# Optimization experiments

Hardware: AMD Instinct MI355X
Metric: run time of the kernel (lower is better)

## Reference

```python
import jax, jax.numpy as jnp
import numpy as np

IM_SIZE = (256, 256)
OVERSAMP = 1.25
WIDTH = 6
BETA = float(np.pi * np.sqrt((WIDTH / OVERSAMP * (OVERSAMP - 0.5)) ** 2 - 0.8))
OS_SIZE = tuple(int(np.ceil(OVERSAMP * n)) for n in IM_SIZE)  # (320, 320)
D = 2


def _kb(x):
    # Kaiser-Bessel interpolation kernel: i0(beta*sqrt(1-x^2)) for |x|<=1 (sigpy convention)
    return jnp.i0(BETA * jnp.sqrt(jnp.maximum(1.0 - x * x, 0.0)))


def setup_inputs() -> dict:
    key = jax.random.key(0)
    k1, k2, k3 = jax.random.split(key, 3)
    N, C = 1, 8
    img_r = jax.random.normal(k1, (N, C) + IM_SIZE, dtype=jnp.float32)
    img_i = jax.random.normal(k2, (N, C) + IM_SIZE, dtype=jnp.float32)
    # trajectory in [-N_i/2, N_i/2] per the class docstring
    trj = (jax.random.uniform(k3, (N, 64, 4096, D), dtype=jnp.float32) - 0.5) * 256.0
    return {"img_r": img_r, "img_i": img_i, "trj": trj}


def _nufft_forward(img_r, img_i, trj):
    img = (img_r + 1j * img_i).astype(jnp.complex64)  # (N, C, H, W)
    nd = img.ndim
    # --- apodization (inverse FT of KB kernel), separable per axis ---
    for a in range(D):
        n, osn = IM_SIZE[a], OS_SIZE[a]
        idx = jnp.arange(n, dtype=jnp.float32)
        arg = jnp.sqrt(BETA ** 2 - (np.pi * WIDTH * (idx - n // 2) / osn) ** 2)
        apod = arg / jnp.sinh(arg)
        shape = [1] * nd
        shape[nd - D + a] = n
        img = img * apod.reshape(shape)
    # --- scale + centered zero-pad to oversampled grid ---
    img = img / np.sqrt(float(np.prod(IM_SIZE)))
    pads = [(0, 0)] * (nd - D) + [(((o - n) // 2), (o - n) - ((o - n) // 2))
                                  for n, o in zip(IM_SIZE, OS_SIZE)]
    img = jnp.pad(img, pads)
    # --- centered FFT (ifftshift -> fftn(norm=None) -> fftshift) ---
    axes = tuple(range(-D, 0))
    ksp_os = jnp.fft.fftshift(jnp.fft.fftn(jnp.fft.ifftshift(img, axes=axes), axes=axes), axes=axes)
    # --- scale trajectory to oversampled grid coordinates ---
    scale = jnp.array([OS_SIZE[a] / IM_SIZE[a] for a in range(D)], jnp.float32)
    shift = jnp.array([OS_SIZE[a] // 2 for a in range(D)], jnp.float32)
    coord = trj * scale + shift  # (N, R, S, 2)
    x0 = jnp.ceil(coord - WIDTH / 2.0)
    # --- KB interpolation: fixed 6x6 neighbor loop, vectorized gather over all points ---
    N = img.shape[0]
    out = jnp.zeros((N,) + img.shape[1:nd - D] + coord.shape[1:-1], jnp.complex64)

    def gather(grid, ix, iy):  # grid (C, Hos, Wos), ix/iy (R, S) -> (C, R, S)
        return grid[:, ix, iy]

    for dx in range(WIDTH):
        px = x0[..., 0] + dx
        wx = _kb((px - coord[..., 0]) / (WIDTH / 2.0))
        ix = px.astype(jnp.int32) % OS_SIZE[0]
        for dy in range(WIDTH):
            py = x0[..., 1] + dy
            wy = _kb((py - coord[..., 1]) / (WIDTH / 2.0))
            iy = py.astype(jnp.int32) % OS_SIZE[1]
            vals = jax.vmap(gather)(ksp_os, ix, iy)  # (N, C, R, S)
            out = out + vals * (wx * wy)[:, None, :, :]
    return out / (WIDTH ** D)


def reference(img_r, img_i, trj):
    return _nufft_forward(img_r, img_i, trj)
```

## Files before the change

### kernel.cpp

```cpp
#include <hip/hip_runtime.h>
#include <math.h>

#define NCH   8
#define IMN   256
#define OSN   320
#define NPTS  (64*4096)
#define KD    512
#define BETA_F   10.9551078f
#define BETA2_F  120.014389f
#define APOD_C   0.05890486225f

typedef unsigned short u16;
typedef unsigned int   u32;
typedef __attribute__((ext_vector_type(8))) short s16x8;
typedef __attribute__((ext_vector_type(4))) float f32x4;
typedef __attribute__((ext_vector_type(2))) float f32x2;

__device__ __forceinline__ u32 f2bf(float f) {
    u32 u = __float_as_uint(f);
    return (u + 0x7FFFu + ((u >> 16) & 1u)) >> 16;
}

__device__ __forceinline__ float i0f(float t) {
    if (t < 3.75f) {
        float y = t * t * (1.0f / 14.0625f);
        return 1.0f + y * (3.5156229f + y * (3.0899424f + y * (1.2067492f +
                     y * (0.2659732f + y * (0.0360768f + y * 0.0045813f)))));
    }
    float z = 3.75f / t;
    float p = 0.39894228f + z * (0.01328592f + z * (0.00225319f + z * (-0.00157565f +
              z * (0.00916281f + z * (-0.02057706f + z * (0.02635537f +
              z * (-0.01647633f + z * 0.00392377f)))))));
    return expf(t) * rsqrtf(t) * p;
}

__device__ __forceinline__ float apodf(int i) {
    float x = APOD_C * (float)(i - IMN / 2);
    float arg = sqrtf(BETA2_F - x * x);
    float e = expf(arg);
    float sh = 0.5f * (e - 1.0f / e);
    return arg / sh;
}

__global__ void prep(const float* __restrict__ r, const float* __restrict__ im,
                     u32* __restrict__ B1, u32* __restrict__ B2,
                     u32* __restrict__ A) {
    const int b = blockIdx.x, t = threadIdx.x;
    if (b < (OSN * IMN) / 256) {
        int idx = b * 256 + t;
        int k = idx >> 8, j = idx & 255;
        int p = (k * (j + 32)) % OSN;
        float th = (2.0f * (float)M_PI / (float)OSN) * (float)p;
        float s = ((k + j) & 1) ? -1.0f : 1.0f;
        float sn, cs;
        sincosf(th, &sn, &cs);
        float re = s * cs, imv = -s * sn;
        B1[idx] = f2bf(re) | (f2bf(-imv) << 16);
        B2[idx] = f2bf(imv) | (f2bf(re) << 16);
    } else {
        int idx = (b - (OSN * IMN) / 256) * 256 + t;
        int i2 = idx & 255, i1 = (idx >> 8) & 255;
        float w = apodf(i1) * apodf(i2) * (1.0f / 256.0f);
        A[idx] = f2bf(r[idx] * w) | (f2bf(im[idx] * w) << 16);
    }
}

__launch_bounds__(64)
__global__ void gemm1(const short* __restrict__ Abf, const short* __restrict__ B1,
                      const short* __restrict__ B2, short* __restrict__ Tb) {
    const int c = blockIdx.z;
    const int mBase = blockIdx.y * 32;
    const int nBase = blockIdx.x * 32;
    __shared__ short As[2][32][36], B1s[2][32][36], B2s[2][32][36];
    const int t = threadIdx.x;
    const int row = t >> 1, seg = (t & 1) * 16;
    const int fm = t & 15, fq = (t >> 4) * 8;
    const short* ap  = Abf + (long)(c * IMN + mBase + row) * KD + seg;
    const short* b1p = B1 + (long)(nBase + row) * KD + seg;
    const short* b2p = B2 + (long)(nBase + row) * KD + seg;
    f32x4 zz = {0.f, 0.f, 0.f, 0.f};
    f32x4 accRe[2][2], accIm[2][2];
    #pragma unroll
    for (int i = 0; i < 2; i++)
        #pragma unroll
        for (int j = 0; j < 2; j++) { accRe[i][j] = zz; accIm[i][j] = zz; }

    s16x8 c0 = *(const s16x8*)(ap);
    s16x8 c1 = *(const s16x8*)(ap + 8);
    s16x8 c2 = *(const s16x8*)(b1p);
    s16x8 c3 = *(const s16x8*)(b1p + 8);
    s16x8 c4 = *(const s16x8*)(b2p);
    s16x8 c5 = *(const s16x8*)(b2p + 8);

    #pragma unroll
    for (int kc = 0; kc < 16; kc++) {
        const int buf = kc & 1;
        *(s16x8*)&As [buf][row][seg]     = c0;
        *(s16x8*)&As [buf][row][seg + 8] = c1;
        *(s16x8*)&B1s[buf][row][seg]     = c2;
        *(s16x8*)&B1s[buf][row][seg + 8] = c3;
        *(s16x8*)&B2s[buf][row][seg]     = c4;
        *(s16x8*)&B2s[buf][row][seg + 8] = c5;
        if (kc < 15) {
            const int kb = (kc + 1) * 32;
            c0 = *(const s16x8*)(ap + kb);
            c1 = *(const s16x8*)(ap + kb + 8);
            c2 = *(const s16x8*)(b1p + kb);
            c3 = *(const s16x8*)(b1p + kb + 8);
            c4 = *(const s16x8*)(b2p + kb);
            c5 = *(const s16x8*)(b2p + kb + 8);
        }
        s16x8 a0  = *(const s16x8*)&As [buf][fm][fq];
        s16x8 a1  = *(const s16x8*)&As [buf][16 + fm][fq];
        s16x8 b10 = *(const s16x8*)&B1s[buf][fm][fq];
        s16x8 b11 = *(const s16x8*)&B1s[buf][16 + fm][fq];
        s16x8 b20 = *(const s16x8*)&B2s[buf][fm][fq];
        s16x8 b21 = *(const s16x8*)&B2s[buf][16 + fm][fq];
        accRe[0][0] = __builtin_amdgcn_mfma_f32_16x16x32_bf16(a0, b10, accRe[0][0], 0, 0, 0);
        accRe[0][1] = __builtin_amdgcn_mfma_f32_16x16x32_bf16(a0, b11, accRe[0][1], 0, 0, 0);
        accRe[1][0] = __builtin_amdgcn_mfma_f32_16x16x32_bf16(a1, b10, accRe[1][0], 0, 0, 0);
        accRe[1][1] = __builtin_amdgcn_mfma_f32_16x16x32_bf16(a1, b11, accRe[1][1], 0, 0, 0);
        accIm[0][0] = __builtin_amdgcn_mfma_f32_16x16x32_bf16(a0, b20, accIm[0][0], 0, 0, 0);
        accIm[0][1] = __builtin_amdgcn_mfma_f32_16x16x32_bf16(a0, b21, accIm[0][1], 0, 0, 0);
        accIm[1][0] = __builtin_amdgcn_mfma_f32_16x16x32_bf16(a1, b20, accIm[1][0], 0, 0, 0);
        accIm[1][1] = __builtin_amdgcn_mfma_f32_16x16x32_bf16(a1, b21, accIm[1][1], 0, 0, 0);
    }
    #pragma unroll
    for (int i = 0; i < 2; i++)
        #pragma unroll
        for (int j = 0; j < 2; j++) {
            int i1b = mBase + i * 16 + (t >> 4) * 4;
            int k2  = nBase + j * 16 + fm;
            s16x8 v;
            #pragma unroll
            for (int r = 0; r < 4; r++) {
                v[2 * r]     = (short)f2bf(accRe[i][j][r]);
                v[2 * r + 1] = (short)f2bf(accIm[i][j][r]);
            }
            *(s16x8*)(Tb + ((long)(c * OSN + k2)) * KD + 2 * i1b) = v;
        }
}

__launch_bounds__(64)
__global__ void gemm2(const short* __restrict__ B1, const short* __restrict__ B2,
                      const short* __restrict__ Tb, u32* __restrict__ Gb) {
    const int c = blockIdx.z;
    const int mBase = blockIdx.y * 32;
    const int nBase = blockIdx.x * 32;
    __shared__ short A1s[2][32][36], A2s[2][32][36], Bs[2][32][36];
    const int t = threadIdx.x;
    const int row = t >> 1, seg = (t & 1) * 16;
    const int fm = t & 15, fq = (t >> 4) * 8;
    const short* a1p = B1 + (long)(mBase + row) * KD + seg;
    const short* a2p = B2 + (long)(mBase + row) * KD + seg;
    const short* bp  = Tb + ((long)(c * OSN + nBase + row)) * KD + seg;
    f32x4 zz = {0.f, 0.f, 0.f, 0.f};
    f32x4 accRe[2][2], accIm[2][2];
    #pragma unroll
    for (int i = 0; i < 2; i++)
        #pragma unroll
        for (int j = 0; j < 2; j++) { accRe[i][j] = zz; accIm[i][j] = zz; }

    s16x8 c0 = *(const s16x8*)(a1p);
    s16x8 c1 = *(const s16x8*)(a1p + 8);
    s16x8 c2 = *(const s16x8*)(a2p);
    s16x8 c3 = *(const s16x8*)(a2p + 8);
    s16x8 c4 = *(const s16x8*)(bp);
    s16x8 c5 = *(const s16x8*)(bp + 8);

    #pragma unroll
    for (int kc = 0; kc < 16; kc++) {
        const int buf = kc & 1;
        *(s16x8*)&A1s[buf][row][seg]     = c0;
        *(s16x8*)&A1s[buf][row][seg + 8] = c1;
        *(s16x8*)&A2s[buf][row][seg]     = c2;
        *(s16x8*)&A2s[buf][row][seg + 8] = c3;
        *(s16x8*)&Bs [buf][row][seg]     = c4;
        *(s16x8*)&Bs [buf][row][seg + 8] = c5;
        if (kc < 15) {
            const int kb = (kc + 1) * 32;
            c0 = *(const s16x8*)(a1p + kb);
            c1 = *(const s16x8*)(a1p + kb + 8);
            c2 = *(const s16x8*)(a2p + kb);
            c3 = *(const s16x8*)(a2p + kb + 8);
            c4 = *(const s16x8*)(bp + kb);
            c5 = *(const s16x8*)(bp + kb + 8);
        }
        s16x8 a10 = *(const s16x8*)&A1s[buf][fm][fq];
        s16x8 a11 = *(const s16x8*)&A1s[buf][16 + fm][fq];
        s16x8 a20 = *(const s16x8*)&A2s[buf][fm][fq];
        s16x8 a21 = *(const s16x8*)&A2s[buf][16 + fm][fq];
        s16x8 b0  = *(const s16x8*)&Bs [buf][fm][fq];
        s16x8 b1  = *(const s16x8*)&Bs [buf][16 + fm][fq];
        accRe[0][0] = __builtin_amdgcn_mfma_f32_16x16x32_bf16(a10, b0, accRe[0][0], 0, 0, 0);
        accRe[0][1] = __builtin_amdgcn_mfma_f32_16x16x32_bf16(a10, b1, accRe[0][1], 0, 0, 0);
        accRe[1][0] = __builtin_amdgcn_mfma_f32_16x16x32_bf16(a11, b0, accRe[1][0], 0, 0, 0);
        accRe[1][1] = __builtin_amdgcn_mfma_f32_16x16x32_bf16(a11, b1, accRe[1][1], 0, 0, 0);
        accIm[0][0] = __builtin_amdgcn_mfma_f32_16x16x32_bf16(a20, b0, accIm[0][0], 0, 0, 0);
        accIm[0][1] = __builtin_amdgcn_mfma_f32_16x16x32_bf16(a20, b1, accIm[0][1], 0, 0, 0);
        accIm[1][0] = __builtin_amdgcn_mfma_f32_16x16x32_bf16(a21, b0, accIm[1][0], 0, 0, 0);
        accIm[1][1] = __builtin_amdgcn_mfma_f32_16x16x32_bf16(a21, b1, accIm[1][1], 0, 0, 0);
    }
    #pragma unroll
    for (int i = 0; i < 2; i++)
        #pragma unroll
        for (int j = 0; j < 2; j++) {
            int k2 = nBase + j * 16 + fm;
            #pragma unroll
            for (int r = 0; r < 4; r++) {
                int k1 = mBase + i * 16 + (t >> 4) * 4 + r;
                Gb[((long)k1 * OSN + k2) * NCH + c] =
                    f2bf(accRe[i][j][r]) | (f2bf(accIm[i][j][r]) << 16);
            }
        }
}

__global__ void interp_kernel(const float* __restrict__ trj,
                              const u32* __restrict__ grid,
                              u32* __restrict__ out) {
    const int t = threadIdx.x;
    __shared__ float wxs[128][6], wys[128][6];
    __shared__ int   x0s[128], y0s[128];

    {
        int ptl = t & 127, axis = t >> 7;
        int pt = blockIdx.x * 128 + ptl;
        float tv = trj[pt * 2 + axis];
        float cc = __fadd_rn(__fmul_rn(tv, 1.25f), 160.0f);
        float v0 = ceilf(__fadd_rn(cc, -3.0f));
        if (axis) y0s[ptl] = (int)v0; else x0s[ptl] = (int)v0;
        float* ws = axis ? wys[ptl] : wxs[ptl];
        #pragma unroll
        for (int d = 0; d < 6; d++) {
            float u = __fdiv_rn(__fsub_rn(v0 + (float)d, cc), 3.0f);
            ws[d] = i0f(BETA_F * sqrtf(fmaxf(1.0f - u * u, 0.0f)));
        }
    }
    __syncthreads();

    const int pl = t >> 1;
    const int h = (t & 1) * 4;
    int rb[6], iyb[6];
    float wx[6], wy[6];
    const int x0i = x0s[pl], y0i = y0s[pl];
    #pragma unroll
    for (int d = 0; d < 6; d++) {
        int vx = x0i + d;
        if (vx < 0) vx += OSN;
        if (vx >= OSN) vx -= OSN;
        rb[d] = vx * (OSN * NCH) + h;
        int vy = y0i + d;
        if (vy < 0) vy += OSN;
        if (vy >= OSN) vy -= OSN;
        iyb[d] = vy * NCH;
        wx[d] = wxs[pl][d];
        wy[d] = wys[pl][d];
    }

    f32x2 a0 = {0.f, 0.f}, a1 = {0.f, 0.f}, a2 = {0.f, 0.f}, a3 = {0.f, 0.f};
    #pragma unroll
    for (int dx = 0; dx < 6; dx++) {
        const u32* gp = grid + rb[dx];
        float wxv = wx[dx];
        #pragma unroll
        for (int dy = 0; dy < 6; dy++) {
            uint4 g = *(const uint4*)(gp + iyb[dy]);
            float ww = wxv * wy[dy];
            f32x2 w2 = {ww, ww};
            f32x2 v0v = { __uint_as_float(g.x << 16), __uint_as_float(g.x & 0xFFFF0000u) };
            f32x2 v1v = { __uint_as_float(g.y << 16), __uint_as_float(g.y & 0xFFFF0000u) };
            f32x2 v2v = { __uint_as_float(g.z << 16), __uint_as_float(g.z & 0xFFFF0000u) };
            f32x2 v3v = { __uint_as_float(g.w << 16), __uint_as_float(g.w & 0xFFFF0000u) };
            a0 += v0v * w2;
            a1 += v1v * w2;
            a2 += v2v * w2;
            a3 += v3v * w2;
        }
    }
    f32x2 sc = {1.0f / 36.0f, 1.0f / 36.0f};
    a0 *= sc; a1 *= sc; a2 *= sc; a3 *= sc;

    __shared__ f32x2 lds[128][8];
    lds[pl][h]     = a0;
    lds[pl][h + 1] = a1;
    lds[pl][h + 2] = a2;
    lds[pl][h + 3] = a3;
    __syncthreads();
    int c2 = t >> 5, p2 = t & 31;
    long ob = (long)c2 * NPTS + blockIdx.x * 128;
    #pragma unroll
    for (int k = 0; k < 4; k++) {
        f32x2 v = lds[p2 + 32 * k][c2];
        out[ob + p2 + 32 * k] = f2bf(v.y) | (f2bf(v.x) << 16);
    }
}

extern "C" void kernel_launch(void* const* d_in, const int* in_sizes, int n_in,
                              void* d_out, int out_size, void* d_ws, size_t ws_size,
                              hipStream_t stream) {
    const float* img_r = (const float*)d_in[0];
    const float* img_i = (const float*)d_in[1];
    const float* trj   = (const float*)d_in[2];

    char* ob = (char*)d_out;
    short* Tb  = (short*)(ob);
    u32*  B1u  = (u32*)(ob + 2621440);
    u32*  B2u  = (u32*)(ob + 2949120);
    u32*  Au   = (u32*)(ob + 3276800);
    u32*  Gb   = (u32*)d_ws;

    prep<<<(OSN * IMN) / 256 + (NCH * IMN * IMN) / 256, 256, 0, stream>>>(
        img_r, img_i, B1u, B2u, Au);
    gemm1<<<dim3(OSN / 32, IMN / 32, NCH), 64, 0, stream>>>(
        (const short*)Au, (const short*)B1u, (const short*)B2u, Tb);
    gemm2<<<dim3(OSN / 32, OSN / 32, NCH), 64, 0, stream>>>(
        (const short*)B1u, (const short*)B2u, Tb, Gb);
    interp_kernel<<<NPTS / 128, 256, 0, stream>>>(trj, Gb, (u32*)d_out);
}
```

Measured before the change: 119.4 us.

## Pad oversampled grid with wrap halo and prefetch interpolation rows

The FFT output is now written into a padded grid of 326x328 that carries a 3-cell wrap-around halo, with boundary values duplicated. The interpolation kernel can then address neighbours linearly without modulo wraparound or per-tap index arrays. Loads for the next x-row are double-buffered in registers, and the LDS transpose buffer is padded to avoid bank conflicts. The cost is extra boundary stores in the FFT kernel, a larger workspace, and higher register pressure from the 12 uint4 buffers.

```diff
diff --git a/kernel.cpp b/kernel.cpp
--- a/kernel.cpp
+++ b/kernel.cpp
@@ -9,6 +9,9 @@
 #define BETA_F   10.9551078f
 #define BETA2_F  120.014389f
 #define APOD_C   0.05890486225f
+#define GROWS 326
+#define GCOLS 328
+#define GPITCH (GCOLS * NCH)
 
 typedef unsigned short u16;
 typedef unsigned int   u32;
@@ -206,11 +209,18 @@
         #pragma unroll
         for (int j = 0; j < 2; j++) {
             int k2 = nBase + j * 16 + fm;
+            int pc  = k2 + 3;
+            int pc2 = (k2 < 3) ? (k2 + 323) : ((k2 >= 317) ? (k2 - 317) : -1);
             #pragma unroll
             for (int r = 0; r < 4; r++) {
                 int k1 = mBase + i * 16 + (t >> 4) * 4 + r;
-                Gb[((long)k1 * OSN + k2) * NCH + c] =
-                    f2bf(accRe[i][j][r]) | (f2bf(accIm[i][j][r]) << 16);
+                u32 val = f2bf(accRe[i][j][r]) | (f2bf(accIm[i][j][r]) << 16);
+                int pr  = k1 + 3;
+                int pr2 = (k1 < 3) ? (k1 + 323) : ((k1 >= 317) ? (k1 - 317) : -1);
+                Gb[(long)pr * GPITCH + pc * NCH + c] = val;
+                if (pr2 >= 0)              Gb[(long)pr2 * GPITCH + pc  * NCH + c] = val;
+                if (pc2 >= 0)              Gb[(long)pr  * GPITCH + pc2 * NCH + c] = val;
+                if (pr2 >= 0 && pc2 >= 0)  Gb[(long)pr2 * GPITCH + pc2 * NCH + c] = val;
             }
         }
 }
@@ -239,32 +249,31 @@
     __syncthreads();
 
     const int pl = t >> 1;
-    const int h = (t & 1) * 4;
-    int rb[6], iyb[6];
+    const int h = t & 1;
     float wx[6], wy[6];
-    const int x0i = x0s[pl], y0i = y0s[pl];
-    #pragma unroll
-    for (int d = 0; d < 6; d++) {
-        int vx = x0i + d;
-        if (vx < 0) vx += OSN;
-        if (vx >= OSN) vx -= OSN;
-        rb[d] = vx * (OSN * NCH) + h;
-        int vy = y0i + d;
-        if (vy < 0) vy += OSN;
-        if (vy >= OSN) vy -= OSN;
-        iyb[d] = vy * NCH;
-        wx[d] = wxs[pl][d];
-        wy[d] = wys[pl][d];
-    }
+    #pragma unroll
+    for (int d = 0; d < 6; d++) { wx[d] = wxs[pl][d]; wy[d] = wys[pl][d]; }
+    const int px = x0s[pl] + 3;
+    const int py = y0s[pl] + 3;
+    const u32* g0 = grid + (long)px * GPITCH + py * NCH + h * 4;
+
+    uint4 buf[2][6];
+    #pragma unroll
+    for (int dy = 0; dy < 6; dy++) buf[0][dy] = *(const uint4*)(g0 + dy * NCH);
 
     f32x2 a0 = {0.f, 0.f}, a1 = {0.f, 0.f}, a2 = {0.f, 0.f}, a3 = {0.f, 0.f};
     #pragma unroll
     for (int dx = 0; dx < 6; dx++) {
-        const u32* gp = grid + rb[dx];
+        if (dx < 5) {
+            const u32* gn = g0 + (dx + 1) * GPITCH;
+            #pragma unroll
+            for (int dy = 0; dy < 6; dy++)
+                buf[(dx + 1) & 1][dy] = *(const uint4*)(gn + dy * NCH);
+        }
         float wxv = wx[dx];
         #pragma unroll
         for (int dy = 0; dy < 6; dy++) {
-            uint4 g = *(const uint4*)(gp + iyb[dy]);
+            uint4 g = buf[dx & 1][dy];
             float ww = wxv * wy[dy];
             f32x2 w2 = {ww, ww};
             f32x2 v0v = { __uint_as_float(g.x << 16), __uint_as_float(g.x & 0xFFFF0000u) };
@@ -280,11 +289,11 @@
     f32x2 sc = {1.0f / 36.0f, 1.0f / 36.0f};
     a0 *= sc; a1 *= sc; a2 *= sc; a3 *= sc;
 
-    __shared__ f32x2 lds[128][8];
-    lds[pl][h]     = a0;
-    lds[pl][h + 1] = a1;
-    lds[pl][h + 2] = a2;
-    lds[pl][h + 3] = a3;
+    __shared__ f32x2 lds[128][9];
+    lds[pl][h * 4]     = a0;
+    lds[pl][h * 4 + 1] = a1;
+    lds[pl][h * 4 + 2] = a2;
+    lds[pl][h * 4 + 3] = a3;
     __syncthreads();
     int c2 = t >> 5, p2 = t & 31;
     long ob = (long)c2 * NPTS + blockIdx.x * 128;
```

Measured after the change: 115.9 us. 1.03x faster.
